# Kernel tuning notes

Hardware: AMD Instinct MI355X
Metric: run time of the kernel (lower is better)

The kernel has to match this reference:

```python
import jax, jax.numpy as jnp
import numpy as np

N_SAMPLES = 4194304
N_RAYS = 65536


def setup_inputs() -> dict:
    key = jax.random.key(0)
    k1, k2, k3 = jax.random.split(key, 3)
    rgb_samples = jax.random.uniform(k1, (N_SAMPLES, 3), dtype=jnp.float32)
    weights_samples = jax.random.uniform(k2, (N_SAMPLES, 1), dtype=jnp.float32)
    ray_indices = jnp.sort(jax.random.randint(k3, (N_SAMPLES,), 0, N_RAYS, dtype=jnp.int32))
    return {
        "rgb_samples": rgb_samples,
        "weights_samples": weights_samples,
        "ray_indices": ray_indices,
        "n_rays": N_RAYS,
    }


def reference(rgb_samples, weights_samples, ray_indices, n_rays):
    # Packed/ragged per-ray weighted color integration:
    # pred_rgb[r] = sum_{i in ray r} weights[i] * rgb[i]
    weighted = rgb_samples * weights_samples  # [N_samples, 3]
    pred_rgb = jax.ops.segment_sum(weighted, ray_indices, num_segments=n_rays)  # [N_rays, 3]
    return pred_rgb
```

## Files before the change

kernel.cpp:

```cpp
#include <hip/hip_runtime.h>


#define SPL 8
#define WAVE_SAMPLES (64 * SPL)
#define TPW 2

struct Tile {
    int   ids[SPL];
    float ws[SPL], sx[SPL], sy[SPL], sz[SPL];
};

__device__ __forceinline__ void load_tile(const float* __restrict__ rgb,
                                          const float* __restrict__ w,
                                          const int*   __restrict__ idx,
                                          long long tbase, int lane, int n,
                                          Tile& T)
{
    const long long base = tbase + (long long)lane * SPL;
    if (base + SPL <= n) {
        int4   i0 = *(const int4*)(idx + base);
        int4   i1 = *(const int4*)(idx + base + 4);
        float4 w0 = *(const float4*)(w + base);
        float4 w1 = *(const float4*)(w + base + 4);
        const float4* r4 = (const float4*)(rgb + 3 * base);
        float4 r0 = r4[0], r1 = r4[1], r2 = r4[2];
        float4 r3 = r4[3], r4v = r4[4], r5 = r4[5];

        T.ids[0]=i0.x; T.ids[1]=i0.y; T.ids[2]=i0.z; T.ids[3]=i0.w;
        T.ids[4]=i1.x; T.ids[5]=i1.y; T.ids[6]=i1.z; T.ids[7]=i1.w;
        T.ws[0]=w0.x; T.ws[1]=w0.y; T.ws[2]=w0.z; T.ws[3]=w0.w;
        T.ws[4]=w1.x; T.ws[5]=w1.y; T.ws[6]=w1.z; T.ws[7]=w1.w;
        T.sx[0]=r0.x;  T.sy[0]=r0.y;  T.sz[0]=r0.z;
        T.sx[1]=r0.w;  T.sy[1]=r1.x;  T.sz[1]=r1.y;
        T.sx[2]=r1.z;  T.sy[2]=r1.w;  T.sz[2]=r2.x;
        T.sx[3]=r2.y;  T.sy[3]=r2.z;  T.sz[3]=r2.w;
        T.sx[4]=r3.x;  T.sy[4]=r3.y;  T.sz[4]=r3.z;
        T.sx[5]=r3.w;  T.sy[5]=r4v.x; T.sz[5]=r4v.y;
        T.sx[6]=r4v.z; T.sy[6]=r4v.w; T.sz[6]=r5.x;
        T.sx[7]=r5.y;  T.sy[7]=r5.z;  T.sz[7]=r5.w;
    } else {
        #pragma unroll
        for (int k = 0; k < SPL; ++k) {
            long long s  = base + k;
            bool      ok = (s < n);
            long long sc = ok ? s : (long long)(n - 1);
            T.ids[k] = idx[sc];
            T.ws[k]  = ok ? w[sc] : 0.0f;
            T.sx[k] = rgb[3*sc+0]; T.sy[k] = rgb[3*sc+1]; T.sz[k] = rgb[3*sc+2];
        }
    }
}

__device__ __forceinline__ void process_tile(const Tile& T, int lane,
                                             float* __restrict__ out)
{
    const int first = T.ids[0];
    int   cur = first;
    float ax = T.ws[0]*T.sx[0], ay = T.ws[0]*T.sy[0], az = T.ws[0]*T.sz[0];
    float hx = 0.f, hy = 0.f, hz = 0.f;
    bool  f = false;
    #pragma unroll
    for (int k = 1; k < SPL; ++k) {
        if (T.ids[k] != cur) {
            if (!f) { hx = ax; hy = ay; hz = az; f = true; }
            else {
                atomicAdd(&out[cur*3+0], ax);
                atomicAdd(&out[cur*3+1], ay);
                atomicAdd(&out[cur*3+2], az);
            }
            ax = ay = az = 0.f;
            cur = T.ids[k];
        }
        ax = fmaf(T.ws[k], T.sx[k], ax);
        ay = fmaf(T.ws[k], T.sy[k], ay);
        az = fmaf(T.ws[k], T.sz[k], az);
    }
    const int t_id = cur;

    int  t_prev = __shfl_up(t_id, 1);
    bool brk    = f || (lane > 0 && t_prev != first);
    unsigned long long bm = __ballot(brk);

    float Sx = ax, Sy = ay, Sz = az;
    #pragma unroll
    for (int d = 1; d < 64; d <<= 1) {
        float ox = __shfl_down(Sx, d);
        float oy = __shfl_down(Sy, d);
        float oz = __shfl_down(Sz, d);
        unsigned long long between = ((bm >> 1) >> lane) & ((1ull << d) - 1ull);
        bool cont = (lane + d < 64) && (between == 0);
        if (cont) { Sx += ox; Sy += oy; Sz += oz; }
    }

    if (lane == 0 || brk) {
        atomicAdd(&out[t_id*3+0], Sx);
        atomicAdd(&out[t_id*3+1], Sy);
        atomicAdd(&out[t_id*3+2], Sz);
    }
    if (f) {
        atomicAdd(&out[first*3+0], hx);
        atomicAdd(&out[first*3+1], hy);
        atomicAdd(&out[first*3+2], hz);
    }
}

__global__ __launch_bounds__(256, 4) void integrate_kernel(
    const float* __restrict__ rgb,
    const float* __restrict__ w,
    const int*   __restrict__ idx,
    float*       __restrict__ out,
    int n)
{
    const int lane = threadIdx.x & 63;
    const long long wave = ((long long)blockIdx.x * blockDim.x + threadIdx.x) >> 6;
    const long long b0 = wave * (TPW * (long long)WAVE_SAMPLES);
    if (b0 >= n) return;
    const long long b1 = b0 + WAVE_SAMPLES;

    Tile T0, T1;
    const bool has1 = (b1 < n);
    load_tile(rgb, w, idx, b0, lane, n, T0);
    if (has1) load_tile(rgb, w, idx, b1, lane, n, T1);

    process_tile(T0, lane, out);
    if (has1) process_tile(T1, lane, out);
}

extern "C" void kernel_launch(void* const* d_in, const int* in_sizes, int n_in,
                              void* d_out, int out_size, void* d_ws, size_t ws_size,
                              hipStream_t stream) {
    const float* rgb = (const float*)d_in[0];
    const float* w   = (const float*)d_in[1];
    const int*   idx = (const int*)  d_in[2];
    float*       out = (float*)d_out;

    int n = in_sizes[2];

    hipMemsetAsync(d_out, 0, (size_t)out_size * sizeof(float), stream);

    long long tiles  = ((long long)n + WAVE_SAMPLES - 1) / WAVE_SAMPLES;
    long long waves  = (tiles + TPW - 1) / TPW;
    long long blocks = (waves + 3) / 4;
    integrate_kernel<<<(int)blocks, 256, 0, stream>>>(rgb, w, idx, out, n);
}
```

Before: 110.0 us.

## Replace interior segment atomics with plain stores, merge tile boundary partials

Segments that lie entirely inside a wave's tile are now written with plain stores instead of atomicAdd. Only the first and last partial segments of each tile are reported to lane 0, which merges them across the wave's two tiles and issues atomics only for segments that may cross wave boundaries. This cuts the atomic traffic to global memory. In exchange it adds extra shuffles and a serial, branchy lane-0 epilogue, and correctness depends on the head/tail classification being exact.

```diff
diff --git a/kernel.cpp b/kernel.cpp
--- a/kernel.cpp
+++ b/kernel.cpp
@@ -8,6 +8,12 @@
 struct Tile {
     int   ids[SPL];
     float ws[SPL], sx[SPL], sy[SPL], sz[SPL];
+};
+
+struct TileOut {
+    int   fid, lid;
+    float Px, Py, Pz;
+    float Tx, Ty, Tz;
 };
 
 __device__ __forceinline__ void load_tile(const float* __restrict__ rgb,
@@ -52,7 +58,8 @@
 }
 
 __device__ __forceinline__ void process_tile(const Tile& T, int lane,
-                                             float* __restrict__ out)
+                                             float* __restrict__ out,
+                                             TileOut& R)
 {
     const int first = T.ids[0];
     int   cur = first;
@@ -64,9 +71,7 @@
         if (T.ids[k] != cur) {
             if (!f) { hx = ax; hy = ay; hz = az; f = true; }
             else {
-                atomicAdd(&out[cur*3+0], ax);
-                atomicAdd(&out[cur*3+1], ay);
-                atomicAdd(&out[cur*3+2], az);
+                out[cur*3+0] = ax; out[cur*3+1] = ay; out[cur*3+2] = az;
             }
             ax = ay = az = 0.f;
             cur = T.ids[k];
@@ -78,7 +83,8 @@
     const int t_id = cur;
 
     int  t_prev = __shfl_up(t_id, 1);
-    bool brk    = f || (lane > 0 && t_prev != first);
+    bool edge   = (lane > 0) && (t_prev != first);
+    bool brk    = f || edge;
     unsigned long long bm = __ballot(brk);
 
     float Sx = ax, Sy = ay, Sz = az;
@@ -92,16 +98,34 @@
         if (cont) { Sx += ox; Sy += oy; Sz += oz; }
     }
 
-    if (lane == 0 || brk) {
-        atomicAdd(&out[t_id*3+0], Sx);
-        atomicAdd(&out[t_id*3+1], Sy);
-        atomicAdd(&out[t_id*3+2], Sz);
-    }
-    if (f) {
-        atomicAdd(&out[first*3+0], hx);
-        atomicAdd(&out[first*3+1], hy);
-        atomicAdd(&out[first*3+2], hz);
-    }
+    const unsigned long long HM = bm | 1ull;
+    const int h_last = 63 - __builtin_clzll(HM);
+
+    unsigned long long above = (lane < 63) ? (HM >> (lane + 1)) : 0ull;
+    int  L  = above ? (lane + 1 + __builtin_ctzll(above)) : 64;
+    int  Ls = (L < 64) ? L : 0;
+    bool my_absorbed = f && (lane > 0) && !edge;
+    int   absL = __shfl((int)my_absorbed, Ls);
+    float ahx  = __shfl(hx, Ls), ahy = __shfl(hy, Ls), ahz = __shfl(hz, Ls);
+    bool  doAbs = (L < 64) && absL;
+    float Vx = Sx + (doAbs ? ahx : 0.f);
+    float Vy = Sy + (doAbs ? ahy : 0.f);
+    float Vz = Sz + (doAbs ? ahz : 0.f);
+
+    bool head = (lane == 0) || brk;
+    bool isT  = (lane == h_last);
+    if (head && !isT && !(lane == 0 && !f)) {
+        out[t_id*3+0] = Vx; out[t_id*3+1] = Vy; out[t_id*3+2] = Vz;
+    }
+    if (f && (lane > 0) && edge) {
+        out[first*3+0] = hx; out[first*3+1] = hy; out[first*3+2] = hz;
+    }
+
+    float pvx = f ? hx : Vx, pvy = f ? hy : Vy, pvz = f ? hz : Vz;
+    R.fid = __shfl(first, 0);
+    R.lid = __shfl(t_id, 63);
+    R.Px  = __shfl(pvx, 0); R.Py = __shfl(pvy, 0); R.Pz = __shfl(pvz, 0);
+    R.Tx  = __shfl(Vx, h_last); R.Ty = __shfl(Vy, h_last); R.Tz = __shfl(Vz, h_last);
 }
 
 __global__ __launch_bounds__(256, 4) void integrate_kernel(
@@ -116,14 +140,96 @@
     const long long b0 = wave * (TPW * (long long)WAVE_SAMPLES);
     if (b0 >= n) return;
     const long long b1 = b0 + WAVE_SAMPLES;
+    const bool has1 = (b1 < n);
 
     Tile T0, T1;
-    const bool has1 = (b1 < n);
     load_tile(rgb, w, idx, b0, lane, n, T0);
     if (has1) load_tile(rgb, w, idx, b1, lane, n, T1);
 
-    process_tile(T0, lane, out);
-    if (has1) process_tile(T1, lane, out);
+    TileOut R0, R1;
+    process_tile(T0, lane, out, R0);
+    if (has1) process_tile(T1, lane, out, R1);
+
+    if (lane == 0) {
+        bool s0 = (R0.fid == R0.lid);
+        if (!has1) {
+            atomicAdd(&out[R0.fid*3+0], R0.Px);
+            atomicAdd(&out[R0.fid*3+1], R0.Py);
+            atomicAdd(&out[R0.fid*3+2], R0.Pz);
+            if (!s0) {
+                atomicAdd(&out[R0.lid*3+0], R0.Tx);
+                atomicAdd(&out[R0.lid*3+1], R0.Ty);
+                atomicAdd(&out[R0.lid*3+2], R0.Tz);
+            }
+        } else {
+            bool s1 = (R1.fid == R1.lid);
+            if (s0 && s1) {
+                if (R0.fid == R1.fid) {
+                    atomicAdd(&out[R0.fid*3+0], R0.Px + R1.Px);
+                    atomicAdd(&out[R0.fid*3+1], R0.Py + R1.Py);
+                    atomicAdd(&out[R0.fid*3+2], R0.Pz + R1.Pz);
+                } else {
+                    atomicAdd(&out[R0.fid*3+0], R0.Px);
+                    atomicAdd(&out[R0.fid*3+1], R0.Py);
+                    atomicAdd(&out[R0.fid*3+2], R0.Pz);
+                    atomicAdd(&out[R1.fid*3+0], R1.Px);
+                    atomicAdd(&out[R1.fid*3+1], R1.Py);
+                    atomicAdd(&out[R1.fid*3+2], R1.Pz);
+                }
+            } else if (s0) {
+                if (R0.fid == R1.fid) {
+                    atomicAdd(&out[R0.fid*3+0], R0.Px + R1.Px);
+                    atomicAdd(&out[R0.fid*3+1], R0.Py + R1.Py);
+                    atomicAdd(&out[R0.fid*3+2], R0.Pz + R1.Pz);
+                } else {
+                    atomicAdd(&out[R0.fid*3+0], R0.Px);
+                    atomicAdd(&out[R0.fid*3+1], R0.Py);
+                    atomicAdd(&out[R0.fid*3+2], R0.Pz);
+                    out[R1.fid*3+0] = R1.Px;
+                    out[R1.fid*3+1] = R1.Py;
+                    out[R1.fid*3+2] = R1.Pz;
+                }
+                atomicAdd(&out[R1.lid*3+0], R1.Tx);
+                atomicAdd(&out[R1.lid*3+1], R1.Ty);
+                atomicAdd(&out[R1.lid*3+2], R1.Tz);
+            } else if (s1) {
+                atomicAdd(&out[R0.fid*3+0], R0.Px);
+                atomicAdd(&out[R0.fid*3+1], R0.Py);
+                atomicAdd(&out[R0.fid*3+2], R0.Pz);
+                if (R0.lid == R1.fid) {
+                    atomicAdd(&out[R0.lid*3+0], R0.Tx + R1.Px);
+                    atomicAdd(&out[R0.lid*3+1], R0.Ty + R1.Py);
+                    atomicAdd(&out[R0.lid*3+2], R0.Tz + R1.Pz);
+                } else {
+                    out[R0.lid*3+0] = R0.Tx;
+                    out[R0.lid*3+1] = R0.Ty;
+                    out[R0.lid*3+2] = R0.Tz;
+                    atomicAdd(&out[R1.fid*3+0], R1.Px);
+                    atomicAdd(&out[R1.fid*3+1], R1.Py);
+                    atomicAdd(&out[R1.fid*3+2], R1.Pz);
+                }
+            } else {
+                atomicAdd(&out[R0.fid*3+0], R0.Px);
+                atomicAdd(&out[R0.fid*3+1], R0.Py);
+                atomicAdd(&out[R0.fid*3+2], R0.Pz);
+                if (R0.lid == R1.fid) {
+                    out[R0.lid*3+0] = R0.Tx + R1.Px;
+                    out[R0.lid*3+1] = R0.Ty + R1.Py;
+                    out[R0.lid*3+2] = R0.Tz + R1.Pz;
+                } else {
+                    out[R0.lid*3+0] = R0.Tx;
+                    out[R0.lid*3+1] = R0.Ty;
+                    out[R0.lid*3+2] = R0.Tz;
+                    out[R1.fid*3+0] = R1.Px;
+                    out[R1.fid*3+1] = R1.Py;
+                    out[R1.fid*3+2] = R1.Pz;
+                }
+                atomicAdd(&out[R1.lid*3+0], R1.Tx);
+                atomicAdd(&out[R1.lid*3+1], R1.Ty);
+                atomicAdd(&out[R1.lid*3+2], R1.Tz);
+            }
+        }
+    }
 }
 
 extern "C" void kernel_launch(void* const* d_in, const int* in_sizes, int n_in,
```

Result: slower. 114.9 us (+4.5%).
